# Optimization experiments

Measured on AMD Instinct MI355X. Metric: run time of the kernel, lower is better.

Reference implementation:

```python
import jax, jax.numpy as jnp
import numpy as np

B, T, D, K, DEPTH = 8, 1024, 128, 64, 1


def _rel_ids(T, k):
    # relative_mat_id[i, j] = clamp(k + j - i, 0, 2k)
    base = jnp.arange(k, k + T)[None, :] - jnp.arange(T)[:, None]
    return jnp.clip(base, 0, 2 * k)  # [T, T] int32


def setup_inputs() -> dict:
    key = jax.random.key(0)
    ks = jax.random.split(key, 13)
    s = 1.0 / np.sqrt(D)
    return {
        "x": jax.random.normal(ks[0], (B, T, D), dtype=jnp.float32),
        "W0": jax.random.normal(ks[1], (D, D), dtype=jnp.float32) * s,
        "b0": jnp.zeros((D,), dtype=jnp.float32),
        "Wq": jax.random.normal(ks[2], (D, D), dtype=jnp.float32) * s,
        "bq": jnp.zeros((D,), dtype=jnp.float32),
        "Wk": jax.random.normal(ks[3], (D, D), dtype=jnp.float32) * s,
        "bk": jnp.zeros((D,), dtype=jnp.float32),
        "Wv": jax.random.normal(ks[4], (D, D), dtype=jnp.float32) * s,
        "bv": jnp.zeros((D,), dtype=jnp.float32),
        "W1": jax.random.normal(ks[5], (D, D), dtype=jnp.float32) * s,
        "b1": jnp.zeros((D,), dtype=jnp.float32),
        "pe_key": jax.random.normal(ks[6], (2 * K + 1, D), dtype=jnp.float32) * np.sqrt(2.0 / (2 * K + 1)),
        "pe_value": jax.random.normal(ks[7], (2 * K + 1, D), dtype=jnp.float32) * np.sqrt(2.0 / (2 * K + 1)),
    }


def reference(x, W0, b0, Wq, bq, Wk, bk, Wv, bv, W1, b1, pe_key, pe_value):
    Tlen = x.shape[1]
    ids = _rel_ids(Tlen, K)                     # [T, T]
    rpr_key = pe_key[ids]                       # [T, T, D]
    rpr_value = pe_value[ids]                   # [T, T, D]

    hs = jax.nn.relu(x @ W0 + b0)               # fc0 (dropout = eval identity)
    for _ in range(DEPTH):
        q = jnp.tanh(hs @ Wq + bq)
        k = jnp.tanh(hs @ Wk + bk)
        v = jnp.tanh(hs @ Wv + bv)
        a = jnp.einsum("bid,bjd->bij", q, k)
        a = a + jnp.einsum("ijd,bid->bij", rpr_key, q)
        a = jax.nn.softmax(a, axis=2)
        c = jnp.einsum("bij,bjd->bid", a, v)
        c = c + jnp.einsum("bij,ijd->bid", a, rpr_value)
        hs = jax.nn.relu(c @ W1 + b1)
    return hs
```

## Files before the change

kernel.cpp:

```cpp
#include <hip/hip_runtime.h>


#define TT 1024
#define DD 128
#define NB 8
#define SJH 1160

typedef _Float16 f16;
typedef __attribute__((ext_vector_type(8))) _Float16 f16x8;
typedef __attribute__((ext_vector_type(4))) _Float16 f16x4;
typedef __attribute__((ext_vector_type(4))) float f32x4;

static __device__ inline float fast_tanh(float x) {
    float xc = fminf(fmaxf(x, -12.f), 12.f);
    float e = __expf(2.f * xc);
    return (e - 1.f) / (e + 1.f);
}

__global__ __launch_bounds__(256) void prep_w(
        const float* __restrict__ W0, const float* __restrict__ Wq,
        const float* __restrict__ Wk, const float* __restrict__ Wv,
        const float* __restrict__ W1, f16* __restrict__ wt) {
    const int blk = blockIdx.x, t = threadIdx.x;
    const float* W = blk == 0 ? W0 : blk == 1 ? Wq : blk == 2 ? Wk
                   : blk == 3 ? Wv : W1;
    f16* o = wt + (size_t)blk * 16384;
    for (int it = 0; it < 64; it++) {
        int idx = t + 256 * it;
        int n = idx >> 7, k2 = idx & 127;
        o[n * 128 + k2] = (f16)W[k2 * 128 + n];
    }
}

#define STAGEW(s) do { const char* _src = (const char*)(wt + (size_t)(s) * 16384); \
    _Pragma("unroll") for (int _i = 0; _i < 8; _i++) { \
        int _a = t * 128 + _i * 16; uint4 _d = *(const uint4*)(_src + _a); \
        *(uint4*)(wl + (_a ^ (((_a >> 8) & 7) << 4))) = _d; } } while (0)

#define ZACC() do { _Pragma("unroll") for (int _i = 0; _i < 2; _i++) \
    _Pragma("unroll") for (int _j = 0; _j < 2; _j++) \
        acc[_i][_j] = (f32x4){0.f, 0.f, 0.f, 0.f}; } while (0)

#define GEMMCORE(SRC) do { \
    _Pragma("unroll") for (int _c = 0; _c < 4; _c++) { \
        f16x8 _af[2], _bf[2]; \
        _Pragma("unroll") for (int _it = 0; _it < 2; _it++) { \
            int _row = _it * 16 + (l & 15); \
            int _a = (_row << 8) + (_c << 6) + ((l >> 4) << 4); \
            _af[_it] = *(const f16x8*)((SRC) + (_a ^ ((_row & 7) << 4))); } \
        _Pragma("unroll") for (int _nt = 0; _nt < 2; _nt++) { \
            int _n = wv * 32 + _nt * 16 + (l & 15); \
            int _a = (_n << 8) + (_c << 6) + ((l >> 4) << 4); \
            _bf[_nt] = *(const f16x8*)(wl + (_a ^ ((_n & 7) << 4))); } \
        _Pragma("unroll") for (int _it = 0; _it < 2; _it++) \
        _Pragma("unroll") for (int _nt = 0; _nt < 2; _nt++) \
            acc[_it][_nt] = __builtin_amdgcn_mfma_f32_16x16x32_f16( \
                    _af[_it], _bf[_nt], acc[_it][_nt], 0, 0, 0); } } while (0)

__global__ __launch_bounds__(256) void fused_qkv(
        const float* __restrict__ x, const f16* __restrict__ wt,
        const float* __restrict__ b0, const float* __restrict__ bq,
        const float* __restrict__ bk, const float* __restrict__ bv,
        const float* __restrict__ PEK, const float* __restrict__ PEV,
        f16* __restrict__ q16, char* __restrict__ kimg,
        char* __restrict__ vimg, char* __restrict__ pekimg,
        char* __restrict__ pevimg) {
    __shared__ __align__(16) char lds[49152];
    char* xs  = lds;
    char* hsl = lds + 8192;
    char* wl  = lds + 16384;
    const int t = threadIdx.x, wv = t >> 6, l = t & 63;
    const int blk = blockIdx.x;

    if (blk >= 256) {
        if (blk == 256) {
            for (int it = 0; it < 64; it++) {
                int idx = t + 256 * it;
                int m = idx >> 7, d = idx & 127;
                *(f16*)(pekimg + m * 256 + ((2 * d) ^ ((m & 7) << 4))) =
                        (f16)PEK[m * 128 + d];
            }
        } else {
            for (int it = 0; it < 64; it++) {
                int idx = t + 256 * it;
                int m = idx >> 7, d = idx & 127;
                *(f16*)(pevimg + d * 256 + ((2 * m) ^ ((d & 7) << 4))) =
                        (f16)PEV[m * 128 + d];
            }
        }
        return;
    }

    const int r0 = blk * 32;
    {
        const float* X = x + (size_t)r0 * 128;
        #pragma unroll
        for (int i = 0; i < 2; i++) {
            f32x4 a0 = *(const f32x4*)(X + t * 16 + i * 8);
            f32x4 a1 = *(const f32x4*)(X + t * 16 + i * 8 + 4);
            f16x8 h;
            h[0]=(f16)a0[0]; h[1]=(f16)a0[1]; h[2]=(f16)a0[2]; h[3]=(f16)a0[3];
            h[4]=(f16)a1[0]; h[5]=(f16)a1[1]; h[6]=(f16)a1[2]; h[7]=(f16)a1[3];
            int a = t * 32 + i * 16;
            *(f16x8*)(xs + (a ^ (((a >> 8) & 7) << 4))) = h;
        }
    }
    STAGEW(0);
    __syncthreads();

    f32x4 acc[2][2];
    ZACC();
    GEMMCORE(xs);
    __syncthreads();
    {
        #pragma unroll
        for (int it = 0; it < 2; it++)
            #pragma unroll
            for (int nt = 0; nt < 2; nt++) {
                int n = wv * 32 + nt * 16 + (l & 15);
                float bb = b0[n];
                #pragma unroll
                for (int r = 0; r < 4; r++) {
                    int i = it * 16 + (l >> 4) * 4 + r;
                    float v = fmaxf(acc[it][nt][r] + bb, 0.f);
                    int a = i * 256 + 2 * n;
                    *(f16*)(hsl + (a ^ ((i & 7) << 4))) = (f16)v;
                }
            }
    }
    STAGEW(1);
    __syncthreads();

    ZACC();
    GEMMCORE(hsl);
    {
        #pragma unroll
        for (int it = 0; it < 2; it++)
            #pragma unroll
            for (int nt = 0; nt < 2; nt++) {
                int n = wv * 32 + nt * 16 + (l & 15);
                float bb = bq[n];
                #pragma unroll
                for (int r = 0; r < 4; r++) {
                    int i = it * 16 + (l >> 4) * 4 + r;
                    q16[(size_t)(r0 + i) * 128 + n] =
                            (f16)fast_tanh(acc[it][nt][r] + bb);
                }
            }
    }
    __syncthreads();
    STAGEW(2);
    __syncthreads();

    ZACC();
    GEMMCORE(hsl);
    __syncthreads();
    f16* ts = (f16*)xs;
    {
        #pragma unroll
        for (int it = 0; it < 2; it++)
            #pragma unroll
            for (int nt = 0; nt < 2; nt++) {
                int n = wv * 32 + nt * 16 + (l & 15);
                float bb = bk[n];
                #pragma unroll
                for (int r = 0; r < 4; r++) {
                    int i = it * 16 + (l >> 4) * 4 + r;
                    ts[i * 128 + n] = (f16)fast_tanh(acc[it][nt][r] + bb);
                }
            }
    }
    STAGEW(3);
    __syncthreads();
    {
        #pragma unroll
        for (int half = 0; half < 2; half++) {
            int row = (t >> 4) + half * 16;
            int seg = t & 15;
            int jg = r0 + row;
            int chunk = ((jg >> 10) << 3) + ((jg & 1023) >> 7);
            int jp = jg & 127;
            char* dst = kimg + (size_t)chunk * 32768 + jp * 256
                      + ((seg * 16) ^ ((jp & 7) << 4));
            *(f16x8*)dst = *(const f16x8*)&ts[row * 128 + seg * 8];
        }
    }
    ZACC();
    GEMMCORE(hsl);
    {
        #pragma unroll
        for (int it = 0; it < 2; it++)
            #pragma unroll
            for (int nt = 0; nt < 2; nt++) {
                int d = wv * 32 + nt * 16 + (l & 15);
                float bb = bv[d];
                f16x4 h;
                #pragma unroll
                for (int r = 0; r < 4; r++)
                    h[r] = (f16)fast_tanh(acc[it][nt][r] + bb);
                int jb = r0 + it * 16 + ((l >> 4) << 2);
                int chunk = ((jb >> 10) << 3) + ((jb & 1023) >> 7);
                char* dst = vimg + (size_t)chunk * 32768 + d * 256
                          + ((2 * (jb & 127)) ^ ((d & 7) << 4));
                *(f16x4*)dst = h;
            }
    }
}

#define ISSUE32(src, bi) do { const char* _g = (src) + t * 16; \
    char* _d = BUF + (bi) * 32768 + t * 16; \
    _Pragma("unroll") for (int _i = 0; _i < 4; _i++) \
        __builtin_amdgcn_global_load_lds( \
            (const __attribute__((address_space(1))) unsigned*)(_g + _i * 8192), \
            (__attribute__((address_space(3))) unsigned*)(_d + _i * 8192), 16, 0, 0); \
} while (0)

__global__ __launch_bounds__(512) void attn_all(
        const f16* __restrict__ q16, const char* __restrict__ kimg,
        const char* __restrict__ pekimg, const char* __restrict__ vimg,
        const char* __restrict__ pevimg, const float* __restrict__ PEK,
        const float* __restrict__ PEV, const f16* __restrict__ w1t,
        const float* __restrict__ b1, float* __restrict__ out) {
    extern __shared__ __align__(16) char sm6[];
    f16*   S   = (f16*)sm6;
    char*  BUF = sm6 + 74240;
    f16*   QB  = (f16*)(sm6 + 74240 + 65536);
    float* LR  = (float*)(sm6 + 74240 + 65536 + 8448);

    const int t = threadIdx.x, wv = t >> 6, l = t & 63;
    const int lr = l & 15, lg = l >> 4;
    const int b = blockIdx.x & 7;
    const int i0 = (blockIdx.x >> 3) << 5;
    const int it16 = (wv & 1) << 4;
    const int jsub = wv >> 1;

    f16x8 qf[4];
    {
        const f16* qb = q16 + (size_t)(b * TT + i0 + it16 + lr) * 128 + lg * 8;
        #pragma unroll
        for (int c = 0; c < 4; c++) qf[c] = *(const f16x8*)(qb + c * 32);
    }

    const char* kbase = kimg + (size_t)b * 8 * 32768;
    const char* vbase = vimg + (size_t)b * 8 * 32768;

    ISSUE32(kbase, 0);
    for (int ch = 0; ch < 9; ++ch) {
        asm volatile("s_waitcnt vmcnt(0)" ::: "memory");
        __builtin_amdgcn_s_barrier();
        __builtin_amdgcn_sched_barrier(0);
        if (ch < 8)
            ISSUE32(ch < 7 ? kbase + (size_t)(ch + 1) * 32768 : pekimg, (ch + 1) & 1);
        const char* kb = BUF + (ch & 1) * 32768;
        #pragma unroll
        for (int jt = 0; jt < 2; jt++) {
            const int jp = jsub * 32 + jt * 16 + lr;
            f32x4 acc = {0.f, 0.f, 0.f, 0.f};
            #pragma unroll
            for (int c = 0; c < 4; c++) {
                f16x8 kf = *(const f16x8*)(kb + jp * 256
                            + ((c * 64 + lg * 16) ^ ((jp & 7) << 4)));
                acc = __builtin_amdgcn_mfma_f32_16x16x32_f16(kf, qf[c], acc, 0, 0, 0);
            }
            f16x4 h = {(f16)acc[0], (f16)acc[1], (f16)acc[2], (f16)acc[3]};
            *(f16x4*)&S[(it16 + lr) * SJH + ch * 128 + jsub * 32 + jt * 16 + lg * 4] = h;
        }
    }
    asm volatile("s_waitcnt lgkmcnt(0)" ::: "memory");
    __builtin_amdgcn_s_barrier();
    __builtin_amdgcn_sched_barrier(0);
    ISSUE32(vbase, 0);

    {
        const int row = t >> 4, l16 = t & 15;
        const int ig = i0 + row;
        f16* srow = S + row * SJH;
        f16* qrow = QB + row * 132;

        float qp;
        {
            const f16* qr = q16 + (size_t)(b * TT + ig) * 128 + l16 * 8;
            const float* pr = PEK + 128 * 128 + l16 * 8;
            f16x8 qv = *(const f16x8*)qr;
            float s = 0.f;
            #pragma unroll
            for (int e = 0; e < 8; e++) s += (float)qv[e] * pr[e];
            #pragma unroll
            for (int off = 8; off; off >>= 1) s += __shfl_xor(s, off, 64);
            qp = s;
        }
        for (int mm = l16; mm < 128; mm += 16) {
            qrow[mm] = srow[1024 + mm];
            srow[1024 + mm] = (f16)0.f;
        }
        if (l16 == 0) qrow[128] = (f16)qp;
        const float qlo = (float)qrow[0], qhi = qp;

        float lmax = -3.0e38f;
        #pragma unroll
        for (int kk = 0; kk < 8; kk++) {
            int j0 = kk * 128 + l16 * 8;
            f16x8 sv = *(const f16x8*)(srow + j0);
            #pragma unroll
            for (int e = 0; e < 8; e++) {
                int idd = 64 + j0 + e - ig;
                float qv = (idd <= 0) ? qlo : (idd >= 128 ? qhi : (float)qrow[idd]);
                lmax = fmaxf(lmax, (float)sv[e] + qv);
            }
        }
        #pragma unroll
        for (int off = 8; off; off >>= 1) lmax = fmaxf(lmax, __shfl_xor(lmax, off, 64));

        float lsum = 0.f, s0 = 0.f, s1 = 0.f;
        #pragma unroll
        for (int kk = 0; kk < 8; kk++) {
            int j0 = kk * 128 + l16 * 8;
            f16x8 sv = *(const f16x8*)(srow + j0);
            f16x8 pv;
            #pragma unroll
            for (int e = 0; e < 8; e++) {
                int idd = 64 + j0 + e - ig;
                float qv = (idd <= 0) ? qlo : (idd >= 128 ? qhi : (float)qrow[idd]);
                float p = __expf((float)sv[e] + qv - lmax);
                pv[e] = (f16)p;
                lsum += p;
                if (idd <= 0)        s0 += p;
                else if (idd >= 128) s1 += p;
                else                 srow[1024 + idd] = (f16)p;
            }
            *(f16x8*)(srow + j0) = pv;
        }
        #pragma unroll
        for (int off = 8; off; off >>= 1) {
            lsum += __shfl_xor(lsum, off, 64);
            s0   += __shfl_xor(s0,   off, 64);
            s1   += __shfl_xor(s1,   off, 64);
        }
        if (l16 == 0) {
            srow[1024] = (f16)s0;
            srow[1152] = (f16)s1;
            LR[row] = lsum;
        }
    }
    asm volatile("s_waitcnt lgkmcnt(0)" ::: "memory");
    __builtin_amdgcn_s_barrier();
    __builtin_amdgcn_sched_barrier(0);

    f32x4 cacc[2] = {};
    for (int ch = 0; ch < 9; ++ch) {
        asm volatile("s_waitcnt vmcnt(0)" ::: "memory");
        __builtin_amdgcn_s_barrier();
        __builtin_amdgcn_sched_barrier(0);
        if (ch < 8)
            ISSUE32(ch < 7 ? vbase + (size_t)(ch + 1) * 32768 : pevimg, (ch + 1) & 1);
        const char* vb = BUF + (ch & 1) * 32768;
        const int dp = wv * 16 + lr;
        #pragma unroll
        for (int c2 = 0; c2 < 4; c2++) {
            f16x8 vf = *(const f16x8*)(vb + dp * 256
                        + ((c2 * 64 + lg * 16) ^ ((dp & 7) << 4)));
            #pragma unroll
            for (int i2 = 0; i2 < 2; i2++) {
                f16x8 pf = *(const f16x8*)&S[(i2 * 16 + lr) * SJH
                            + ch * 128 + c2 * 32 + lg * 8];
                cacc[i2] = __builtin_amdgcn_mfma_f32_16x16x32_f16(vf, pf, cacc[i2], 0, 0, 0);
            }
        }
    }

    float w128[2], rden[2];
    #pragma unroll
    for (int i2 = 0; i2 < 2; i2++) {
        int irow = i2 * 16 + lr;
        w128[i2] = (float)S[irow * SJH + 1152];
        rden[i2] = 1.f / LR[irow];
    }
    __syncthreads();
    char* cl = (char*)S;
    {
        const float* pvr = PEV + 128 * 128;
        #pragma unroll
        for (int i2 = 0; i2 < 2; i2++) {
            int i = i2 * 16 + lr;
            #pragma unroll
            for (int r = 0; r < 4; r++) {
                int d = wv * 16 + lg * 4 + r;
                float cv = (cacc[i2][r] + w128[i2] * pvr[d]) * rden[i2];
                int a = i * 256 + 2 * d;
                *(f16*)(cl + (a ^ ((i & 7) << 4))) = (f16)cv;
            }
        }
    }
    char* wl4 = BUF;
    {
        const char* src = (const char*)w1t;
        #pragma unroll
        for (int i = 0; i < 4; i++) {
            int a = t * 64 + i * 16;
            uint4 dta = *(const uint4*)(src + a);
            *(uint4*)(wl4 + (a ^ (((a >> 8) & 7) << 4))) = dta;
        }
    }
    __syncthreads();

    f32x4 oacc[2] = {};
    #pragma unroll
    for (int c = 0; c < 4; c++) {
        f16x8 af[2], bf;
        #pragma unroll
        for (int i2 = 0; i2 < 2; i2++) {
            int row = i2 * 16 + lr;
            int a = (row << 8) + (c << 6) + (lg << 4);
            af[i2] = *(const f16x8*)(cl + (a ^ ((row & 7) << 4)));
        }
        {
            int n = wv * 16 + lr;
            int a = (n << 8) + (c << 6) + (lg << 4);
            bf = *(const f16x8*)(wl4 + (a ^ ((n & 7) << 4)));
        }
        #pragma unroll
        for (int i2 = 0; i2 < 2; i2++)
            oacc[i2] = __builtin_amdgcn_mfma_f32_16x16x32_f16(af[i2], bf, oacc[i2], 0, 0, 0);
    }
    {
        int n = wv * 16 + lr;
        float bb = b1[n];
        #pragma unroll
        for (int i2 = 0; i2 < 2; i2++) {
            #pragma unroll
            for (int r = 0; r < 4; r++) {
                int i = i2 * 16 + lg * 4 + r;
                out[(size_t)(b * TT + i0 + i) * DD + n] = fmaxf(oacc[i2][r] + bb, 0.f);
            }
        }
    }
}


extern "C" void kernel_launch(void* const* d_in, const int* in_sizes, int n_in,
                              void* d_out, int out_size, void* d_ws, size_t ws_size,
                              hipStream_t stream) {
    const float* x   = (const float*)d_in[0];
    const float* W0  = (const float*)d_in[1];
    const float* b0  = (const float*)d_in[2];
    const float* Wq  = (const float*)d_in[3];
    const float* bq  = (const float*)d_in[4];
    const float* Wk  = (const float*)d_in[5];
    const float* bk  = (const float*)d_in[6];
    const float* Wv  = (const float*)d_in[7];
    const float* bv  = (const float*)d_in[8];
    const float* W1  = (const float*)d_in[9];
    const float* b1  = (const float*)d_in[10];
    const float* pek = (const float*)d_in[11];
    const float* pev = (const float*)d_in[12];
    float* out = (float*)d_out;

    const size_t NTD = (size_t)NB * TT * DD;
    f16* q16 = (f16*)d_ws;
    f16* wt  = q16 + NTD;
    char* kimg   = (char*)(wt + 5 * 16384);
    char* vimg   = kimg + (size_t)64 * 32768;
    char* pekimg = vimg + (size_t)64 * 32768;
    char* pevimg = pekimg + 32768;

    const int SMEM_ATTN = 74240 + 65536 + 8448 + 128;
    hipFuncSetAttribute(reinterpret_cast<const void*>(attn_all),
                        hipFuncAttributeMaxDynamicSharedMemorySize, SMEM_ATTN);

    hipLaunchKernelGGL(prep_w, dim3(5), dim3(256), 0, stream,
                       W0, Wq, Wk, Wv, W1, wt);
    hipLaunchKernelGGL(fused_qkv, dim3(258), dim3(256), 0, stream,
                       x, wt, b0, bq, bk, bv, pek, pev,
                       q16, kimg, vimg, pekimg, pevimg);
    hipLaunchKernelGGL(attn_all, dim3(256), dim3(512), SMEM_ATTN, stream,
                       q16, kimg, pekimg, vimg, pevimg, pek, pev,
                       wt + 4 * 16384, b1, out);
}
```

Before: 56.49 us.

## Pre-swizzle weights and pipeline K/V tiles with deeper async LDS prefetch

Weights are pre-swizzled in prep_w so fused_qkv can load them straight into LDS with global_load_lds, double-buffered across the four GEMMs instead of staged synchronously between barriers. In attn_all the K/V chunk size drops from 128 to 64 rows with a 4-deep ring buffer and vmcnt-based waits, so loads run several chunks ahead of compute. The W1 tile is also loaded asynchronously, and some per-row constants (q, PE rows, bias) are hoisted into early loads. The cost is more barriers per chunk (18 instead of 9 iterations), more fragile waitcnt bookkeeping, and larger dynamic LDS for fused_qkv, which could lower its occupancy.

```diff
diff --git a/kernel.cpp b/kernel.cpp
--- a/kernel.cpp
+++ b/kernel.cpp
@@ -17,31 +17,31 @@
     return (e - 1.f) / (e + 1.f);
 }
 
+#define GLDS(gp, lp) __builtin_amdgcn_global_load_lds( \
+    (const __attribute__((address_space(1))) unsigned*)(gp), \
+    (__attribute__((address_space(3))) unsigned*)(lp), 16, 0, 0)
+
 __global__ __launch_bounds__(256) void prep_w(
         const float* __restrict__ W0, const float* __restrict__ Wq,
         const float* __restrict__ Wk, const float* __restrict__ Wv,
-        const float* __restrict__ W1, f16* __restrict__ wt) {
+        const float* __restrict__ W1, char* __restrict__ wimg) {
     const int blk = blockIdx.x, t = threadIdx.x;
     const float* W = blk == 0 ? W0 : blk == 1 ? Wq : blk == 2 ? Wk
                    : blk == 3 ? Wv : W1;
-    f16* o = wt + (size_t)blk * 16384;
+    char* o = wimg + (size_t)blk * 32768;
     for (int it = 0; it < 64; it++) {
         int idx = t + 256 * it;
-        int n = idx >> 7, k2 = idx & 127;
-        o[n * 128 + k2] = (f16)W[k2 * 128 + n];
+        int k = idx >> 7, n = idx & 127;
+        int a = n * 256 + 2 * k;
+        *(f16*)(o + (a ^ ((n & 7) << 4))) = (f16)W[k * 128 + n];
     }
 }
-
-#define STAGEW(s) do { const char* _src = (const char*)(wt + (size_t)(s) * 16384); \
-    _Pragma("unroll") for (int _i = 0; _i < 8; _i++) { \
-        int _a = t * 128 + _i * 16; uint4 _d = *(const uint4*)(_src + _a); \
-        *(uint4*)(wl + (_a ^ (((_a >> 8) & 7) << 4))) = _d; } } while (0)
 
 #define ZACC() do { _Pragma("unroll") for (int _i = 0; _i < 2; _i++) \
     _Pragma("unroll") for (int _j = 0; _j < 2; _j++) \
         acc[_i][_j] = (f32x4){0.f, 0.f, 0.f, 0.f}; } while (0)
 
-#define GEMMCORE(SRC) do { \
+#define GEMMCORE(SRC, WL) do { \
     _Pragma("unroll") for (int _c = 0; _c < 4; _c++) { \
         f16x8 _af[2], _bf[2]; \
         _Pragma("unroll") for (int _it = 0; _it < 2; _it++) { \
@@ -51,24 +51,38 @@
         _Pragma("unroll") for (int _nt = 0; _nt < 2; _nt++) { \
             int _n = wv * 32 + _nt * 16 + (l & 15); \
             int _a = (_n << 8) + (_c << 6) + ((l >> 4) << 4); \
-            _bf[_nt] = *(const f16x8*)(wl + (_a ^ ((_n & 7) << 4))); } \
+            _bf[_nt] = *(const f16x8*)((WL) + (_a ^ ((_n & 7) << 4))); } \
         _Pragma("unroll") for (int _it = 0; _it < 2; _it++) \
         _Pragma("unroll") for (int _nt = 0; _nt < 2; _nt++) \
             acc[_it][_nt] = __builtin_amdgcn_mfma_f32_16x16x32_f16( \
                     _af[_it], _bf[_nt], acc[_it][_nt], 0, 0, 0); } } while (0)
 
+#define ISSUEW(wi, dst) do { \
+    const char* _g = wimg + (size_t)(wi) * 32768 + t * 16; \
+    char* _d = (dst) + t * 16; \
+    _Pragma("unroll") for (int _i = 0; _i < 8; _i++) \
+        GLDS(_g + _i * 4096, _d + _i * 4096); \
+} while (0)
+
+#define QKVBAR() do { \
+    asm volatile("s_waitcnt vmcnt(0) lgkmcnt(0)" ::: "memory"); \
+    __builtin_amdgcn_s_barrier(); \
+    __builtin_amdgcn_sched_barrier(0); \
+} while (0)
+
 __global__ __launch_bounds__(256) void fused_qkv(
-        const float* __restrict__ x, const f16* __restrict__ wt,
+        const float* __restrict__ x, const char* __restrict__ wimg,
         const float* __restrict__ b0, const float* __restrict__ bq,
         const float* __restrict__ bk, const float* __restrict__ bv,
         const float* __restrict__ PEK, const float* __restrict__ PEV,
         f16* __restrict__ q16, char* __restrict__ kimg,
         char* __restrict__ vimg, char* __restrict__ pekimg,
         char* __restrict__ pevimg) {
-    __shared__ __align__(16) char lds[49152];
-    char* xs  = lds;
-    char* hsl = lds + 8192;
-    char* wl  = lds + 16384;
+    extern __shared__ __align__(16) char smq[];
+    char* xs  = smq;
+    char* hsl = smq + 8192;
+    char* wA  = smq + 16384;
+    char* wB  = smq + 49152;
     const int t = threadIdx.x, wv = t >> 6, l = t & 63;
     const int blk = blockIdx.x;
 
@@ -77,21 +91,22 @@
             for (int it = 0; it < 64; it++) {
                 int idx = t + 256 * it;
                 int m = idx >> 7, d = idx & 127;
-                *(f16*)(pekimg + m * 256 + ((2 * d) ^ ((m & 7) << 4))) =
-                        (f16)PEK[m * 128 + d];
+                *(f16*)(pekimg + (m >> 6) * 16384 + (m & 63) * 256
+                        + ((2 * d) ^ ((m & 7) << 4))) = (f16)PEK[m * 128 + d];
             }
         } else {
             for (int it = 0; it < 64; it++) {
                 int idx = t + 256 * it;
                 int m = idx >> 7, d = idx & 127;
-                *(f16*)(pevimg + d * 256 + ((2 * m) ^ ((d & 7) << 4))) =
-                        (f16)PEV[m * 128 + d];
+                *(f16*)(pevimg + (m >> 6) * 16384 + d * 128
+                        + ((2 * (m & 63)) ^ ((d & 7) << 4))) = (f16)PEV[m * 128 + d];
             }
         }
         return;
     }
 
     const int r0 = blk * 32;
+    ISSUEW(0, wA);
     {
         const float* X = x + (size_t)r0 * 128;
         #pragma unroll
@@ -105,13 +120,12 @@
             *(f16x8*)(xs + (a ^ (((a >> 8) & 7) << 4))) = h;
         }
     }
-    STAGEW(0);
-    __syncthreads();
+    QKVBAR();
 
     f32x4 acc[2][2];
+    ISSUEW(1, wB);
     ZACC();
-    GEMMCORE(xs);
-    __syncthreads();
+    GEMMCORE(xs, wA);
     {
         #pragma unroll
         for (int it = 0; it < 2; it++)
@@ -128,11 +142,11 @@
                 }
             }
     }
-    STAGEW(1);
-    __syncthreads();
-
+    QKVBAR();
+
+    ISSUEW(2, wA);
     ZACC();
-    GEMMCORE(hsl);
+    GEMMCORE(hsl, wB);
     {
         #pragma unroll
         for (int it = 0; it < 2; it++)
@@ -148,13 +162,11 @@
                 }
             }
     }
-    __syncthreads();
-    STAGEW(2);
-    __syncthreads();
-
+    QKVBAR();
+
+    ISSUEW(3, wB);
     ZACC();
-    GEMMCORE(hsl);
-    __syncthreads();
+    GEMMCORE(hsl, wA);
     f16* ts = (f16*)xs;
     {
         #pragma unroll
@@ -170,23 +182,23 @@
                 }
             }
     }
-    STAGEW(3);
-    __syncthreads();
+    QKVBAR();
+
     {
         #pragma unroll
         for (int half = 0; half < 2; half++) {
             int row = (t >> 4) + half * 16;
             int seg = t & 15;
             int jg = r0 + row;
-            int chunk = ((jg >> 10) << 3) + ((jg & 1023) >> 7);
-            int jp = jg & 127;
-            char* dst = kimg + (size_t)chunk * 32768 + jp * 256
+            int chunk = ((jg >> 10) << 4) + ((jg & 1023) >> 6);
+            int jp = jg & 63;
+            char* dst = kimg + (size_t)chunk * 16384 + jp * 256
                       + ((seg * 16) ^ ((jp & 7) << 4));
             *(f16x8*)dst = *(const f16x8*)&ts[row * 128 + seg * 8];
         }
     }
     ZACC();
-    GEMMCORE(hsl);
+    GEMMCORE(hsl, wB);
     {
         #pragma unroll
         for (int it = 0; it < 2; it++)
@@ -199,33 +211,31 @@
                 for (int r = 0; r < 4; r++)
                     h[r] = (f16)fast_tanh(acc[it][nt][r] + bb);
                 int jb = r0 + it * 16 + ((l >> 4) << 2);
-                int chunk = ((jb >> 10) << 3) + ((jb & 1023) >> 7);
-                char* dst = vimg + (size_t)chunk * 32768 + d * 256
-                          + ((2 * (jb & 127)) ^ ((d & 7) << 4));
+                int chunk = ((jb >> 10) << 4) + ((jb & 1023) >> 6);
+                char* dst = vimg + (size_t)chunk * 16384 + d * 128
+                          + ((2 * (jb & 63)) ^ ((d & 7) << 4));
                 *(f16x4*)dst = h;
             }
     }
 }
 
-#define ISSUE32(src, bi) do { const char* _g = (src) + t * 16; \
-    char* _d = BUF + (bi) * 32768 + t * 16; \
-    _Pragma("unroll") for (int _i = 0; _i < 4; _i++) \
-        __builtin_amdgcn_global_load_lds( \
-            (const __attribute__((address_space(1))) unsigned*)(_g + _i * 8192), \
-            (__attribute__((address_space(3))) unsigned*)(_d + _i * 8192), 16, 0, 0); \
+#define ISSUE16(src, bi) do { const char* _g = (src) + t * 16; \
+    char* _d = BUF + (size_t)(bi) * 16384 + t * 16; \
+    GLDS(_g, _d); \
+    GLDS(_g + 8192, _d + 8192); \
 } while (0)
 
 __global__ __launch_bounds__(512) void attn_all(
         const f16* __restrict__ q16, const char* __restrict__ kimg,
         const char* __restrict__ pekimg, const char* __restrict__ vimg,
         const char* __restrict__ pevimg, const float* __restrict__ PEK,
-        const float* __restrict__ PEV, const f16* __restrict__ w1t,
+        const float* __restrict__ PEV, const char* __restrict__ w1img,
         const float* __restrict__ b1, float* __restrict__ out) {
-    extern __shared__ __align__(16) char sm6[];
-    f16*   S   = (f16*)sm6;
-    char*  BUF = sm6 + 74240;
-    f16*   QB  = (f16*)(sm6 + 74240 + 65536);
-    float* LR  = (float*)(sm6 + 74240 + 65536 + 8448);
+    extern __shared__ __align__(16) char sm7[];
+    f16*   S   = (f16*)sm7;
+    char*  BUF = sm7 + 74240;
+    f16*   QB  = (f16*)(sm7 + 139776);
+    float* LR  = (float*)(sm7 + 148224);
 
     const int t = threadIdx.x, wv = t >> 6, l = t & 63;
     const int lr = l & 15, lg = l >> 4;
@@ -240,51 +250,59 @@
         #pragma unroll
         for (int c = 0; c < 4; c++) qf[c] = *(const f16x8*)(qb + c * 32);
     }
-
-    const char* kbase = kimg + (size_t)b * 8 * 32768;
-    const char* vbase = vimg + (size_t)b * 8 * 32768;
-
-    ISSUE32(kbase, 0);
-    for (int ch = 0; ch < 9; ++ch) {
-        asm volatile("s_waitcnt vmcnt(0)" ::: "memory");
+    const int row2 = t >> 4, l16 = t & 15;
+    f16x8 qpv = *(const f16x8*)(q16 + (size_t)(b * TT + i0 + row2) * 128 + l16 * 8);
+    f32x4 pkv0 = *(const f32x4*)(PEK + 128 * 128 + l16 * 8);
+    f32x4 pkv1 = *(const f32x4*)(PEK + 128 * 128 + l16 * 8 + 4);
+    f32x4 pvr4 = *(const f32x4*)(PEV + 128 * 128 + wv * 16 + lg * 4);
+    const float bb1 = b1[wv * 16 + lr];
+
+    const char* kbase = kimg + (size_t)b * 16 * 16384;
+    const char* vbase = vimg + (size_t)b * 16 * 16384;
+
+    ISSUE16(kbase, 0);
+    ISSUE16(kbase + 16384, 1);
+    ISSUE16(kbase + 2 * 16384, 2);
+
+    for (int ch = 0; ch < 18; ch++) {
+        asm volatile("s_waitcnt vmcnt(4)" ::: "memory");
         __builtin_amdgcn_s_barrier();
         __builtin_amdgcn_sched_barrier(0);
-        if (ch < 8)
-            ISSUE32(ch < 7 ? kbase + (size_t)(ch + 1) * 32768 : pekimg, (ch + 1) & 1);
-        const char* kb = BUF + (ch & 1) * 32768;
-        #pragma unroll
-        for (int jt = 0; jt < 2; jt++) {
-            const int jp = jsub * 32 + jt * 16 + lr;
-            f32x4 acc = {0.f, 0.f, 0.f, 0.f};
-            #pragma unroll
-            for (int c = 0; c < 4; c++) {
-                f16x8 kf = *(const f16x8*)(kb + jp * 256
-                            + ((c * 64 + lg * 16) ^ ((jp & 7) << 4)));
-                acc = __builtin_amdgcn_mfma_f32_16x16x32_f16(kf, qf[c], acc, 0, 0, 0);
-            }
-            f16x4 h = {(f16)acc[0], (f16)acc[1], (f16)acc[2], (f16)acc[3]};
-            *(f16x4*)&S[(it16 + lr) * SJH + ch * 128 + jsub * 32 + jt * 16 + lg * 4] = h;
-        }
+        {
+            int ci = ch + 3;
+            const char* src = ci < 16 ? kbase + (size_t)ci * 16384
+                            : (ci < 18 ? pekimg + (size_t)(ci - 16) * 16384
+                                       : vbase + (size_t)(ci - 18) * 16384);
+            ISSUE16(src, ci & 3);
+        }
+        const char* kb = BUF + (size_t)(ch & 3) * 16384;
+        const int jp = jsub * 16 + lr;
+        f32x4 acc = {0.f, 0.f, 0.f, 0.f};
+        #pragma unroll
+        for (int c = 0; c < 4; c++) {
+            f16x8 kf = *(const f16x8*)(kb + jp * 256
+                        + ((c * 64 + lg * 16) ^ ((jp & 7) << 4)));
+            acc = __builtin_amdgcn_mfma_f32_16x16x32_f16(kf, qf[c], acc, 0, 0, 0);
+        }
+        f16x4 h = {(f16)acc[0], (f16)acc[1], (f16)acc[2], (f16)acc[3]};
+        *(f16x4*)&S[(it16 + lr) * SJH + ch * 64 + jsub * 16 + lg * 4] = h;
     }
     asm volatile("s_waitcnt lgkmcnt(0)" ::: "memory");
     __builtin_amdgcn_s_barrier();
     __builtin_amdgcn_sched_barrier(0);
-    ISSUE32(vbase, 0);
-
-    {
-        const int row = t >> 4, l16 = t & 15;
-        const int ig = i0 + row;
-        f16* srow = S + row * SJH;
-        f16* qrow = QB + row * 132;
+
+    {
+        const int ig = i0 + row2;
+        f16* srow = S + row2 * SJH;
+        f16* qrow = QB + row2 * 132;
 
         float qp;
         {
-            const f16* qr = q16 + (size_t)(b * TT + ig) * 128 + l16 * 8;
-            const float* pr = PEK + 128 * 128 + l16 * 8;
-            f16x8 qv = *(const f16x8*)qr;
             float s = 0.f;
             #pragma unroll
-            for (int e = 0; e < 8; e++) s += (float)qv[e] * pr[e];
+            for (int e = 0; e < 4; e++) s += (float)qpv[e] * pkv0[e];
+            #pragma unroll
+            for (int e = 0; e < 4; e++) s += (float)qpv[e + 4] * pkv1[e];
             #pragma unroll
             for (int off = 8; off; off >>= 1) s += __shfl_xor(s, off, 64);
             qp = s;
@@ -339,7 +357,7 @@
         if (l16 == 0) {
             srow[1024] = (f16)s0;
             srow[1152] = (f16)s1;
-            LR[row] = lsum;
+            LR[row2] = lsum;
         }
     }
     asm volatile("s_waitcnt lgkmcnt(0)" ::: "memory");
@@ -347,22 +365,34 @@
     __builtin_amdgcn_sched_barrier(0);
 
     f32x4 cacc[2] = {};
-    for (int ch = 0; ch < 9; ++ch) {
-        asm volatile("s_waitcnt vmcnt(0)" ::: "memory");
+    for (int ch = 0; ch < 18; ch++) {
+        if (ch <= 15)      asm volatile("s_waitcnt vmcnt(4)" ::: "memory");
+        else if (ch == 16) asm volatile("s_waitcnt vmcnt(2)" ::: "memory");
+        else               asm volatile("s_waitcnt vmcnt(0)" ::: "memory");
         __builtin_amdgcn_s_barrier();
         __builtin_amdgcn_sched_barrier(0);
-        if (ch < 8)
-            ISSUE32(ch < 7 ? vbase + (size_t)(ch + 1) * 32768 : pevimg, (ch + 1) & 1);
-        const char* vb = BUF + (ch & 1) * 32768;
+        if (ch < 15) {
+            int ci = ch + 3;
+            const char* src = ci < 16 ? vbase + (size_t)ci * 16384
+                                      : pevimg + (size_t)(ci - 16) * 16384;
+            ISSUE16(src, (ci + 2) & 3);
+        } else if (ch == 17) {
+            const char* _g = w1img + t * 16;
+            char* _d = BUF + t * 16;
+            #pragma unroll
+            for (int _i = 0; _i < 4; _i++)
+                GLDS(_g + _i * 8192, _d + _i * 8192);
+        }
+        const char* vb = BUF + (size_t)((ch + 2) & 3) * 16384;
         const int dp = wv * 16 + lr;
         #pragma unroll
-        for (int c2 = 0; c2 < 4; c2++) {
-            f16x8 vf = *(const f16x8*)(vb + dp * 256
+        for (int c2 = 0; c2 < 2; c2++) {
+            f16x8 vf = *(const f16x8*)(vb + dp * 128
                         + ((c2 * 64 + lg * 16) ^ ((dp & 7) << 4)));
             #pragma unroll
             for (int i2 = 0; i2 < 2; i2++) {
                 f16x8 pf = *(const f16x8*)&S[(i2 * 16 + lr) * SJH
-                            + ch * 128 + c2 * 32 + lg * 8];
+                            + ch * 64 + c2 * 32 + lg * 8];
                 cacc[i2] = __builtin_amdgcn_mfma_f32_16x16x32_f16(vf, pf, cacc[i2], 0, 0, 0);
             }
         }
@@ -375,34 +405,28 @@
         w128[i2] = (float)S[irow * SJH + 1152];
         rden[i2] = 1.f / LR[irow];
     }
-    __syncthreads();
+    asm volatile("s_waitcnt lgkmcnt(0)" ::: "memory");
+    __builtin_amdgcn_s_barrier();
+    __builtin_amdgcn_sched_barrier(0);
     char* cl = (char*)S;
     {
-        const float* pvr = PEV + 128 * 128;
         #pragma unroll
         for (int i2 = 0; i2 < 2; i2++) {
             int i = i2 * 16 + lr;
             #pragma unroll
             for (int r = 0; r < 4; r++) {
                 int d = wv * 16 + lg * 4 + r;
-                float cv = (cacc[i2][r] + w128[i2] * pvr[d]) * rden[i2];
+                float cv = (cacc[i2][r] + w128[i2] * pvr4[r]) * rden[i2];
                 int a = i * 256 + 2 * d;
                 *(f16*)(cl + (a ^ ((i & 7) << 4))) = (f16)cv;
             }
         }
     }
-    char* wl4 = BUF;
-    {
-        const char* src = (const char*)w1t;
-        #pragma unroll
-        for (int i = 0; i < 4; i++) {
-            int a = t * 64 + i * 16;
-            uint4 dta = *(const uint4*)(src + a);
-            *(uint4*)(wl4 + (a ^ (((a >> 8) & 7) << 4))) = dta;
-        }
-    }
-    __syncthreads();
-
+    asm volatile("s_waitcnt vmcnt(0) lgkmcnt(0)" ::: "memory");
+    __builtin_amdgcn_s_barrier();
+    __builtin_amdgcn_sched_barrier(0);
+
+    const char* wl4 = BUF;
     f32x4 oacc[2] = {};
     #pragma unroll
     for (int c = 0; c < 4; c++) {
@@ -424,13 +448,12 @@
     }
     {
         int n = wv * 16 + lr;
-        float bb = b1[n];
         #pragma unroll
         for (int i2 = 0; i2 < 2; i2++) {
             #pragma unroll
             for (int r = 0; r < 4; r++) {
                 int i = i2 * 16 + lg * 4 + r;
-                out[(size_t)(b * TT + i0 + i) * DD + n] = fmaxf(oacc[i2][r] + bb, 0.f);
+                out[(size_t)(b * TT + i0 + i) * DD + n] = fmaxf(oacc[i2][r] + bb1, 0.f);
             }
         }
     }
@@ -457,22 +480,25 @@
 
     const size_t NTD = (size_t)NB * TT * DD;
     f16* q16 = (f16*)d_ws;
-    f16* wt  = q16 + NTD;
-    char* kimg   = (char*)(wt + 5 * 16384);
-    char* vimg   = kimg + (size_t)64 * 32768;
-    char* pekimg = vimg + (size_t)64 * 32768;
+    char* wimg   = (char*)(q16 + NTD);
+    char* kimg   = wimg + 5 * 32768;
+    char* vimg   = kimg + (size_t)128 * 16384;
+    char* pekimg = vimg + (size_t)128 * 16384;
     char* pevimg = pekimg + 32768;
 
-    const int SMEM_ATTN = 74240 + 65536 + 8448 + 128;
+    const int SMEM_QKV  = 81920;
+    const int SMEM_ATTN = 148352;
+    hipFuncSetAttribute(reinterpret_cast<const void*>(fused_qkv),
+                        hipFuncAttributeMaxDynamicSharedMemorySize, SMEM_QKV);
     hipFuncSetAttribute(reinterpret_cast<const void*>(attn_all),
                         hipFuncAttributeMaxDynamicSharedMemorySize, SMEM_ATTN);
 
     hipLaunchKernelGGL(prep_w, dim3(5), dim3(256), 0, stream,
-                       W0, Wq, Wk, Wv, W1, wt);
-    hipLaunchKernelGGL(fused_qkv, dim3(258), dim3(256), 0, stream,
-                       x, wt, b0, bq, bk, bv, pek, pev,
+                       W0, Wq, Wk, Wv, W1, wimg);
+    hipLaunchKernelGGL(fused_qkv, dim3(258), dim3(256), SMEM_QKV, stream,
+                       x, wimg, b0, bq, bk, bv, pek, pev,
                        q16, kimg, vimg, pekimg, pevimg);
     hipLaunchKernelGGL(attn_all, dim3(256), dim3(512), SMEM_ATTN, stream,
                        q16, kimg, pekimg, vimg, pevimg, pek, pev,
-                       wt + 4 * 16384, b1, out);
+                       wimg + 4 * 32768, b1, out);
 }
```

Result: faster. 53.83 us (-4.7%).
